# Performance work log

Measured on AMD Instinct MI355X. Metric: run time of the kernel, lower is better.

The kernel has to match this reference:

```python
import jax, jax.numpy as jnp
import numpy as np

BINS = 8
EPS = 1e-12  # torch F.normalize default eps


def _pairwise_scores(matf):
    # torch: input1[a,b]=matf[b]; transpose(0,1)->matf[a]; transpose(-2,-1)->matf[a]^T [M,F]
    # matmul with input1[a,b]=matf[b] -> scores[a,b] = matf[a]^T @ matf[b], shape [M,M]
    bs, F, M = matf.shape
    s = jnp.einsum('afm,bfn->abmn', matf, matf)  # [bs, bs, M, M]
    return s.reshape(bs * bs, M * M)


def _histc_rows(x, bins):
    # torch.histc semantics with min=max=0: range = [row.min(), row.max()],
    # values == max land in the last bin.
    mn = jnp.min(x, axis=1, keepdims=True)
    mx = jnp.max(x, axis=1, keepdims=True)
    denom = jnp.where(mx > mn, mx - mn, jnp.ones_like(mx))
    idx = jnp.clip(jnp.floor((x - mn) / denom * bins).astype(jnp.int32), 0, bins - 1)
    nbs = x.shape[0]
    flat = (idx + (jnp.arange(nbs, dtype=jnp.int32) * bins)[:, None]).ravel()
    h = jnp.zeros(nbs * bins, dtype=x.dtype).at[flat].add(1.0)
    return h.reshape(nbs, bins)


def _l2_normalize(h):
    n = jnp.linalg.norm(h, axis=-1, keepdims=True)
    return h / jnp.maximum(n, EPS)


def setup_inputs() -> dict:
    key = jax.random.key(0)
    k1, k2 = jax.random.split(key)
    bs, F, M = 64, 256, 128
    matf1 = jax.random.normal(k1, (bs, F, M), dtype=jnp.float32)
    matf2 = jax.random.normal(k2, (bs, F, M), dtype=jnp.float32)
    return {"matf1": matf1, "matf2": matf2}


def reference(matf1, matf2):
    # scores are .detach()ed in the original; stop_gradient for faithfulness
    scores1 = jax.lax.stop_gradient(_pairwise_scores(matf1))  # [nbs, M*M]
    scores2 = jax.lax.stop_gradient(_pairwise_scores(matf2))
    h1 = _l2_normalize(_histc_rows(scores1, BINS))  # [nbs, 8]
    h2 = _l2_normalize(_histc_rows(scores2, BINS))
    return jnp.concatenate([h1, h2], axis=-1)  # [nbs, 16]
```

## Files before the change

kernel.cpp:

```cpp
#include <hip/hip_runtime.h>
#include <math.h>

#define BS 64
#define F  256
#define M  128
#define MF (M * F)
#define NBP 1056

typedef unsigned short u16;
typedef _Float16 f16x8 __attribute__((ext_vector_type(8)));
typedef float    f32x16 __attribute__((ext_vector_type(16)));

__global__ __launch_bounds__(256) void convert_f16_kernel(
    const float* __restrict__ m1, const float* __restrict__ m2,
    u16* __restrict__ hT)
{
    __shared__ float tile[64 * M];
    const int mat = blockIdx.x >> 6;
    const int b   = blockIdx.x & 63;
    const int f0  = blockIdx.y * 64;
    const float* src = (mat == 0 ? m1 : m2) + (size_t)b * MF + (size_t)f0 * M;
    const int tid = threadIdx.x;

    const float4* g = (const float4*)src;
    float4* s = (float4*)tile;
    #pragma unroll
    for (int i = 0; i < 8; ++i)
        s[tid + i * 256] = g[tid + i * 256];
    __syncthreads();

    const size_t obase = ((size_t)(mat * BS + b) * 32 + (f0 >> 3)) * 1024;
    #pragma unroll
    for (int it = 0; it < 4; ++it) {
        const int idx = it * 256 + tid;
        const int f8l = idx >> 7;
        const int m   = idx & 127;
        u16 hh[8] __attribute__((aligned(16)));
        #pragma unroll
        for (int j = 0; j < 8; ++j) {
            const float x = tile[(f8l * 8 + j) * M + m];
            const _Float16 h = (_Float16)x;
            hh[j] = __builtin_bit_cast(u16, h);
        }
        *(uint4*)&hT[obase + (size_t)idx * 8] = *(const uint4*)hh;
    }
}


#define LOADB(DST, IT) {                                      \
    const u16* pbk = pb + (IT) * 4096;                        \
    DST[0][0] = *(const f16x8*)(pbk);                         \
    DST[0][1] = *(const f16x8*)(pbk + 256);                   \
    DST[1][0] = *(const f16x8*)(pbk + 2048);                  \
    DST[1][1] = *(const f16x8*)(pbk + 2048 + 256);            \
}

#define MFMA_CHUNK(IT, BF) {                                                                        \
    f16x8 af[4];                                                                                    \
    _Pragma("unroll")                                                                               \
    for (int t = 0; t < 4; ++t)                                                                     \
        af[t] = *(const f16x8*)&lds[(IT) * 4096 + t * 256 + abase];                                 \
    _Pragma("unroll")                                                                               \
    for (int ti = 0; ti < 4; ++ti) {                                                                \
        acc[ti][0] = __builtin_amdgcn_mfma_f32_32x32x16_f16(af[ti], BF[0][0], acc[ti][0], 0, 0, 0); \
        acc[ti][1] = __builtin_amdgcn_mfma_f32_32x32x16_f16(af[ti], BF[0][1], acc[ti][1], 0, 0, 0); \
    }                                                                                               \
    _Pragma("unroll")                                                                               \
    for (int t = 0; t < 4; ++t)                                                                     \
        af[t] = *(const f16x8*)&lds[(IT) * 4096 + 2048 + t * 256 + abase];                          \
    _Pragma("unroll")                                                                               \
    for (int ti = 0; ti < 4; ++ti) {                                                                \
        acc[ti][0] = __builtin_amdgcn_mfma_f32_32x32x16_f16(af[ti], BF[1][0], acc[ti][0], 0, 0, 0); \
        acc[ti][1] = __builtin_amdgcn_mfma_f32_32x32x16_f16(af[ti], BF[1][1], acc[ti][1], 0, 0, 0); \
    }                                                                                               \
}

__global__ __launch_bounds__(256, 2) void gram_hist_mfma(
    const u16* __restrict__ hT, float* __restrict__ out)
{
    __shared__ u16 lds[32768];
    __shared__ float smin[4], smax[4];
    __shared__ int hist[2][8];

    const int tid  = threadIdx.x;
    const int lane = tid & 63;
    const int w    = tid >> 6;

    if (tid < 16) hist[tid >> 3][tid & 7] = 0;

    int p = blockIdx.x, a = 0;
    { int cnt = 32; while (p >= cnt) { p -= cnt; ++a; cnt = (64 - a + 1) >> 1; } }
    const int b1 = a + 2 * p;
    int b2 = b1 + 1;
    const bool b2valid = (b2 <= 63);
    if (!b2valid) b2 = b1;
    const int mat = blockIdx.y;

    const int pp = w >> 1;
    const int c  = w & 1;
    const int l31   = lane & 31;
    const int lhalf = lane >> 5;

    const int bsel = pp ? b2 : b1;
    const u16* pb = hT + (size_t)(mat * BS + bsel) * MF
                  + (size_t)(lhalf * 1024 + c * 512 + l31 * 8);

    const u16* pa = hT + (size_t)(mat * BS + a) * MF + tid * 8;

    const int abase = lhalf * 1024 + l31 * 8;

    f32x16 acc[4][2];
    #pragma unroll
    for (int ti = 0; ti < 4; ++ti)
        #pragma unroll
        for (int u = 0; u < 2; ++u)
            #pragma unroll
            for (int r = 0; r < 16; ++r) acc[ti][u][r] = 0.0f;

    f16x8 bA[2][2], bB[2][2];

    LOADB(bA, 0);

    #pragma unroll
    for (int i = 0; i < 16; ++i) {
        const uint4 v = *(const uint4*)(pa + i * 2048);
        *(uint4*)&lds[(tid + i * 256) * 8] = v;
    }
    __syncthreads();

    #pragma unroll
    for (int itp = 0; itp < 4; ++itp) {
        LOADB(bB, 2 * itp + 1);
        MFMA_CHUNK(2 * itp, bA);
        if (itp < 3) LOADB(bA, 2 * itp + 2);
        MFMA_CHUNK(2 * itp + 1, bB);
    }

    float vmin = acc[0][0][0], vmax = vmin;
    #pragma unroll
    for (int ti = 0; ti < 4; ++ti)
        #pragma unroll
        for (int u = 0; u < 2; ++u)
            #pragma unroll
            for (int r = 0; r < 16; ++r) {
                vmin = fminf(vmin, acc[ti][u][r]);
                vmax = fmaxf(vmax, acc[ti][u][r]);
            }
    #pragma unroll
    for (int off = 1; off < 64; off <<= 1) {
        vmin = fminf(vmin, __shfl_xor(vmin, off, 64));
        vmax = fmaxf(vmax, __shfl_xor(vmax, off, 64));
    }
    if (lane == 0) { smin[w] = vmin; smax[w] = vmax; }
    __syncthreads();
    const float pmn = fminf(smin[pp * 2], smin[pp * 2 + 1]);
    const float pmx = fmaxf(smax[pp * 2], smax[pp * 2 + 1]);
    const float denom = (pmx > pmn) ? (pmx - pmn) : 1.0f;
    const float scale = 8.0f / denom;
    const float bias  = -pmn * scale;

    unsigned w0 = 0, w1 = 0;
    #pragma unroll
    for (int ti = 0; ti < 4; ++ti)
        #pragma unroll
        for (int u = 0; u < 2; ++u)
            #pragma unroll
            for (int r = 0; r < 16; ++r) {
                const float t = fmaf(acc[ti][u][r], scale, bias);
                int k = (int)t;
                k = k > 7 ? 7 : k;
                const unsigned inc = 1u << ((k & 3) * 8);
                if (k < 4) w0 += inc; else w1 += inc;
            }
    unsigned e0 = (w0 & 0xFFu)         | (((w0 >> 8)  & 0xFFu) << 16);
    unsigned e1 = ((w0 >> 16) & 0xFFu) | (((w0 >> 24) & 0xFFu) << 16);
    unsigned e2 = (w1 & 0xFFu)         | (((w1 >> 8)  & 0xFFu) << 16);
    unsigned e3 = ((w1 >> 16) & 0xFFu) | (((w1 >> 24) & 0xFFu) << 16);
    #pragma unroll
    for (int off = 32; off > 0; off >>= 1) {
        e0 += __shfl_down(e0, off, 64);
        e1 += __shfl_down(e1, off, 64);
        e2 += __shfl_down(e2, off, 64);
        e3 += __shfl_down(e3, off, 64);
    }
    if (lane == 0) {
        atomicAdd(&hist[pp][0], (int)(e0 & 0xFFFFu)); atomicAdd(&hist[pp][1], (int)(e0 >> 16));
        atomicAdd(&hist[pp][2], (int)(e1 & 0xFFFFu)); atomicAdd(&hist[pp][3], (int)(e1 >> 16));
        atomicAdd(&hist[pp][4], (int)(e2 & 0xFFFFu)); atomicAdd(&hist[pp][5], (int)(e2 >> 16));
        atomicAdd(&hist[pp][6], (int)(e3 & 0xFFFFu)); atomicAdd(&hist[pp][7], (int)(e3 >> 16));
    }
    __syncthreads();

    const int B = (pp == 0) ? b1 : b2;
    const bool valid = (pp == 0) || b2valid;
    if (valid && c == 0 && lane < 8) {
        float ss = 0.0f;
        #pragma unroll
        for (int k = 0; k < 8; ++k) {
            const float cc = (float)hist[pp][k];
            ss += cc * cc;
        }
        const float nrm = fmaxf(sqrtf(ss), 1e-12f);
        const float v = (float)hist[pp][lane] / nrm;
        out[((size_t)a * BS + B) * 16 + mat * 8 + lane] = v;
        if (a != B)
            out[((size_t)B * BS + a) * 16 + mat * 8 + lane] = v;
    }
}

extern "C" void kernel_launch(void* const* d_in, const int* in_sizes, int n_in,
                              void* d_out, int out_size, void* d_ws, size_t ws_size,
                              hipStream_t stream) {
    const float* m1 = (const float*)d_in[0];
    const float* m2 = (const float*)d_in[1];
    float* out = (float*)d_out;

    u16* hT = (u16*)d_ws;

    convert_f16_kernel<<<dim3(128, 4), 256, 0, stream>>>(m1, m2, hT);
    gram_hist_mfma<<<dim3(NBP, 2), 256, 0, stream>>>(hT, out);
}
```

Before: 116.1 us.

## Double-buffer A tile in LDS and overlap its loads with MFMA compute

Replaces the up-front staging of the full 64KB A matrix into LDS with a 4-phase double-buffered pipeline. Each phase holds 16KB, and the next phase's A and B global loads are issued while the current phase's MFMAs run. This cuts LDS use from 64KB to 32KB per block, which may raise occupancy, and hides the initial load latency. It adds per-phase barriers, sched_barrier fences and s_setprio around the MFMA blocks, and the B register double buffer doubles in size, which increases VGPR pressure.

After: 113.2 us. -2.5%, faster.

```diff
diff --git a/kernel.cpp b/kernel.cpp
--- a/kernel.cpp
+++ b/kernel.cpp
@@ -47,38 +47,62 @@
 }
 
 
-#define LOADB(DST, IT) {                                      \
-    const u16* pbk = pb + (IT) * 4096;                        \
-    DST[0][0] = *(const f16x8*)(pbk);                         \
-    DST[0][1] = *(const f16x8*)(pbk + 256);                   \
-    DST[1][0] = *(const f16x8*)(pbk + 2048);                  \
-    DST[1][1] = *(const f16x8*)(pbk + 2048 + 256);            \
-}
-
-#define MFMA_CHUNK(IT, BF) {                                                                        \
-    f16x8 af[4];                                                                                    \
-    _Pragma("unroll")                                                                               \
-    for (int t = 0; t < 4; ++t)                                                                     \
-        af[t] = *(const f16x8*)&lds[(IT) * 4096 + t * 256 + abase];                                 \
-    _Pragma("unroll")                                                                               \
-    for (int ti = 0; ti < 4; ++ti) {                                                                \
-        acc[ti][0] = __builtin_amdgcn_mfma_f32_32x32x16_f16(af[ti], BF[0][0], acc[ti][0], 0, 0, 0); \
-        acc[ti][1] = __builtin_amdgcn_mfma_f32_32x32x16_f16(af[ti], BF[0][1], acc[ti][1], 0, 0, 0); \
-    }                                                                                               \
-    _Pragma("unroll")                                                                               \
-    for (int t = 0; t < 4; ++t)                                                                     \
-        af[t] = *(const f16x8*)&lds[(IT) * 4096 + 2048 + t * 256 + abase];                          \
-    _Pragma("unroll")                                                                               \
-    for (int ti = 0; ti < 4; ++ti) {                                                                \
-        acc[ti][0] = __builtin_amdgcn_mfma_f32_32x32x16_f16(af[ti], BF[1][0], acc[ti][0], 0, 0, 0); \
-        acc[ti][1] = __builtin_amdgcn_mfma_f32_32x32x16_f16(af[ti], BF[1][1], acc[ti][1], 0, 0, 0); \
-    }                                                                                               \
+#define LOADB(DST, P) {                                               \
+    const u16* pbk = pb + (P) * 8192;                                 \
+    DST[0][0][0] = *(const f16x8*)(pbk);                              \
+    DST[0][0][1] = *(const f16x8*)(pbk + 256);                        \
+    DST[0][1][0] = *(const f16x8*)(pbk + 2048);                       \
+    DST[0][1][1] = *(const f16x8*)(pbk + 2048 + 256);                 \
+    DST[1][0][0] = *(const f16x8*)(pbk + 4096);                       \
+    DST[1][0][1] = *(const f16x8*)(pbk + 4096 + 256);                 \
+    DST[1][1][0] = *(const f16x8*)(pbk + 4096 + 2048);                \
+    DST[1][1][1] = *(const f16x8*)(pbk + 4096 + 2048 + 256);          \
+}
+
+#define LOADA(P) {                                                    \
+    const u16* pak = pa + (P) * 8192;                                 \
+    rA0 = *(const uint4*)(pak);                                       \
+    rA1 = *(const uint4*)(pak + 2048);                                \
+    rA2 = *(const uint4*)(pak + 4096);                                \
+    rA3 = *(const uint4*)(pak + 6144);                                \
+}
+
+#define WRITEA(BUF) {                                                 \
+    *(uint4*)&lds[(BUF) + d0]        = rA0;                           \
+    *(uint4*)&lds[(BUF) + 2048 + d0] = rA1;                           \
+    *(uint4*)&lds[(BUF) + 4096 + d0] = rA2;                           \
+    *(uint4*)&lds[(BUF) + 6144 + d0] = rA3;                           \
+}
+
+#define MFMA_P(CUR, BF) {                                                                               \
+    __builtin_amdgcn_s_setprio(1);                                                                      \
+    _Pragma("unroll")                                                                                   \
+    for (int ITl = 0; ITl < 2; ++ITl) {                                                                 \
+        f16x8 af[4];                                                                                    \
+        _Pragma("unroll")                                                                               \
+        for (int t = 0; t < 4; ++t)                                                                     \
+            af[t] = *(const f16x8*)&lds[(CUR) + ITl * 4096 + t * 256 + abase];                          \
+        _Pragma("unroll")                                                                               \
+        for (int ti = 0; ti < 4; ++ti) {                                                                \
+            acc[ti][0] = __builtin_amdgcn_mfma_f32_32x32x16_f16(af[ti], BF[ITl][0][0], acc[ti][0], 0, 0, 0); \
+            acc[ti][1] = __builtin_amdgcn_mfma_f32_32x32x16_f16(af[ti], BF[ITl][0][1], acc[ti][1], 0, 0, 0); \
+        }                                                                                               \
+        _Pragma("unroll")                                                                               \
+        for (int t = 0; t < 4; ++t)                                                                     \
+            af[t] = *(const f16x8*)&lds[(CUR) + ITl * 4096 + 2048 + t * 256 + abase];                   \
+        _Pragma("unroll")                                                                               \
+        for (int ti = 0; ti < 4; ++ti) {                                                                \
+            acc[ti][0] = __builtin_amdgcn_mfma_f32_32x32x16_f16(af[ti], BF[ITl][1][0], acc[ti][0], 0, 0, 0); \
+            acc[ti][1] = __builtin_amdgcn_mfma_f32_32x32x16_f16(af[ti], BF[ITl][1][1], acc[ti][1], 0, 0, 0); \
+        }                                                                                               \
+    }                                                                                                   \
+    __builtin_amdgcn_s_setprio(0);                                                                      \
 }
 
 __global__ __launch_bounds__(256, 2) void gram_hist_mfma(
     const u16* __restrict__ hT, float* __restrict__ out)
 {
-    __shared__ u16 lds[32768];
+    __shared__ u16 lds[2 * 8192];
     __shared__ float smin[4], smax[4];
     __shared__ int hist[2][8];
 
@@ -101,14 +125,15 @@
     const int l31   = lane & 31;
     const int lhalf = lane >> 5;
 
+    const u16* pa = hT + (size_t)(mat * BS + a) * MF + tid * 8;
+    const int d0 = tid * 8;
+
+    const int abase = lhalf * 1024 + l31 * 8;
+
     const int bsel = pp ? b2 : b1;
     const u16* pb = hT + (size_t)(mat * BS + bsel) * MF
                   + (size_t)(lhalf * 1024 + c * 512 + l31 * 8);
 
-    const u16* pa = hT + (size_t)(mat * BS + a) * MF + tid * 8;
-
-    const int abase = lhalf * 1024 + l31 * 8;
-
     f32x16 acc[4][2];
     #pragma unroll
     for (int ti = 0; ti < 4; ++ti)
@@ -117,24 +142,33 @@
             #pragma unroll
             for (int r = 0; r < 16; ++r) acc[ti][u][r] = 0.0f;
 
-    f16x8 bA[2][2], bB[2][2];
+    uint4 rA0, rA1, rA2, rA3;
+    f16x8 bA[2][2][2], bB[2][2][2];
 
     LOADB(bA, 0);
-
-    #pragma unroll
-    for (int i = 0; i < 16; ++i) {
-        const uint4 v = *(const uint4*)(pa + i * 2048);
-        *(uint4*)&lds[(tid + i * 256) * 8] = v;
-    }
-    __syncthreads();
-
-    #pragma unroll
-    for (int itp = 0; itp < 4; ++itp) {
-        LOADB(bB, 2 * itp + 1);
-        MFMA_CHUNK(2 * itp, bA);
-        if (itp < 3) LOADB(bA, 2 * itp + 2);
-        MFMA_CHUNK(2 * itp + 1, bB);
-    }
+    LOADA(0);
+    WRITEA(0);
+    __syncthreads();
+
+    LOADA(1); LOADB(bB, 1);
+    MFMA_P(0, bA);
+    __builtin_amdgcn_sched_barrier(0);
+    WRITEA(8192);
+    __syncthreads();
+
+    LOADA(2); LOADB(bA, 2);
+    MFMA_P(8192, bB);
+    __builtin_amdgcn_sched_barrier(0);
+    WRITEA(0);
+    __syncthreads();
+
+    LOADA(3); LOADB(bB, 3);
+    MFMA_P(0, bA);
+    __builtin_amdgcn_sched_barrier(0);
+    WRITEA(8192);
+    __syncthreads();
+
+    MFMA_P(8192, bB);
 
     float vmin = acc[0][0][0], vmax = vmin;
     #pragma unroll
```

## Tile gram pairs as 2x2 blocks with double-buffered LDS staging

Applied to the files above, without the earlier changes.

Each workgroup now handles a 2x2 tile of batch pairs (row pair ta, column pair tb) with 512 threads, instead of one row against two columns. Both A and B operands are staged through double-buffered LDS slices, so global loads for the next slice overlap with MFMA work on the current one, and each loaded matrix is reused across two pairs. The change also remaps block indices for scheduling and raises MFMA wave priority. The cost is higher LDS use (128KB per block), which may limit occupancy. Diagonal tiles also compute some redundant pairs.

Result: slower. 127.9 us (+10.2%).

```diff
diff --git a/kernel.cpp b/kernel.cpp
--- a/kernel.cpp
+++ b/kernel.cpp
@@ -5,7 +5,7 @@
 #define F  256
 #define M  128
 #define MF (M * F)
-#define NBP 1056
+#define NTILE 528
 
 typedef unsigned short u16;
 typedef _Float16 f16x8 __attribute__((ext_vector_type(8)));
@@ -47,67 +47,86 @@
 }
 
 
-#define LOADB(DST, IT) {                                      \
-    const u16* pbk = pb + (IT) * 4096;                        \
-    DST[0][0] = *(const f16x8*)(pbk);                         \
-    DST[0][1] = *(const f16x8*)(pbk + 256);                   \
-    DST[1][0] = *(const f16x8*)(pbk + 2048);                  \
-    DST[1][1] = *(const f16x8*)(pbk + 2048 + 256);            \
-}
-
-#define MFMA_CHUNK(IT, BF) {                                                                        \
-    f16x8 af[4];                                                                                    \
-    _Pragma("unroll")                                                                               \
-    for (int t = 0; t < 4; ++t)                                                                     \
-        af[t] = *(const f16x8*)&lds[(IT) * 4096 + t * 256 + abase];                                 \
-    _Pragma("unroll")                                                                               \
-    for (int ti = 0; ti < 4; ++ti) {                                                                \
-        acc[ti][0] = __builtin_amdgcn_mfma_f32_32x32x16_f16(af[ti], BF[0][0], acc[ti][0], 0, 0, 0); \
-        acc[ti][1] = __builtin_amdgcn_mfma_f32_32x32x16_f16(af[ti], BF[0][1], acc[ti][1], 0, 0, 0); \
-    }                                                                                               \
-    _Pragma("unroll")                                                                               \
-    for (int t = 0; t < 4; ++t)                                                                     \
-        af[t] = *(const f16x8*)&lds[(IT) * 4096 + 2048 + t * 256 + abase];                          \
-    _Pragma("unroll")                                                                               \
-    for (int ti = 0; ti < 4; ++ti) {                                                                \
-        acc[ti][0] = __builtin_amdgcn_mfma_f32_32x32x16_f16(af[ti], BF[1][0], acc[ti][0], 0, 0, 0); \
-        acc[ti][1] = __builtin_amdgcn_mfma_f32_32x32x16_f16(af[ti], BF[1][1], acc[ti][1], 0, 0, 0); \
-    }                                                                                               \
-}
-
-__global__ __launch_bounds__(256, 2) void gram_hist_mfma(
+#define SLOAD(S) {                                    \
+    const u16* sp = srcp + (S) * 8192;                \
+    sr0 = *(const uint4*)(sp);                        \
+    sr1 = *(const uint4*)(sp + 1024);                 \
+    sr2 = *(const uint4*)(sp + 2048);                 \
+    sr3 = *(const uint4*)(sp + 3072);                 \
+    sr4 = *(const uint4*)(sp + 4096);                 \
+    sr5 = *(const uint4*)(sp + 5120);                 \
+    sr6 = *(const uint4*)(sp + 6144);                 \
+    sr7 = *(const uint4*)(sp + 7168);                 \
+}
+
+#define SWRITE(BUF) {                                 \
+    u16* dp = &lds[dstb + (BUF)];                     \
+    *(uint4*)(dp)        = sr0;                       \
+    *(uint4*)(dp + 1024) = sr1;                       \
+    *(uint4*)(dp + 2048) = sr2;                       \
+    *(uint4*)(dp + 3072) = sr3;                       \
+    *(uint4*)(dp + 4096) = sr4;                       \
+    *(uint4*)(dp + 5120) = sr5;                       \
+    *(uint4*)(dp + 6144) = sr6;                       \
+    *(uint4*)(dp + 7168) = sr7;                       \
+}
+
+#define MFMA_SLICE(BUF) {                                                                             \
+    __builtin_amdgcn_s_setprio(1);                                                                    \
+    _Pragma("unroll")                                                                                 \
+    for (int ITl = 0; ITl < 2; ++ITl) {                                                               \
+        _Pragma("unroll")                                                                             \
+        for (int kk = 0; kk < 2; ++kk) {                                                              \
+            const int base = (BUF) + ITl * 4096 + kk * 2048;                                          \
+            f16x8 af[4], bf[2];                                                                       \
+            _Pragma("unroll")                                                                         \
+            for (int t = 0; t < 4; ++t)                                                               \
+                af[t] = *(const f16x8*)&lds[base + aoffW + t * 256];                                  \
+            bf[0] = *(const f16x8*)&lds[base + boffW];                                                \
+            bf[1] = *(const f16x8*)&lds[base + boffW + 256];                                          \
+            _Pragma("unroll")                                                                         \
+            for (int ti = 0; ti < 4; ++ti) {                                                          \
+                acc[ti][0] = __builtin_amdgcn_mfma_f32_32x32x16_f16(af[ti], bf[0], acc[ti][0], 0, 0, 0); \
+                acc[ti][1] = __builtin_amdgcn_mfma_f32_32x32x16_f16(af[ti], bf[1], acc[ti][1], 0, 0, 0); \
+            }                                                                                         \
+        }                                                                                             \
+    }                                                                                                 \
+    __builtin_amdgcn_s_setprio(0);                                                                    \
+}
+
+__global__ __launch_bounds__(512, 2) void gram_hist_mfma(
     const u16* __restrict__ hT, float* __restrict__ out)
 {
-    __shared__ u16 lds[32768];
-    __shared__ float smin[4], smax[4];
-    __shared__ int hist[2][8];
+    __shared__ u16 lds[4 * 2 * 8192];
+    __shared__ float smin[8], smax[8];
+    __shared__ int hist[4][8];
 
     const int tid  = threadIdx.x;
     const int lane = tid & 63;
     const int w    = tid >> 6;
 
-    if (tid < 16) hist[tid >> 3][tid & 7] = 0;
-
-    int p = blockIdx.x, a = 0;
-    { int cnt = 32; while (p >= cnt) { p -= cnt; ++a; cnt = (64 - a + 1) >> 1; } }
-    const int b1 = a + 2 * p;
-    int b2 = b1 + 1;
-    const bool b2valid = (b2 <= 63);
-    if (!b2valid) b2 = b1;
+    if (tid < 32) hist[tid >> 3][tid & 7] = 0;
+
+    int x = blockIdx.x;
+    x = (x & 7) * 66 + (x >> 3);
+    int tt = x, ta = 0, cnt = 32;
+    while (tt >= cnt) { tt -= cnt; ++ta; cnt = 32 - ta; }
+    const int tb  = ta + tt;
     const int mat = blockIdx.y;
 
-    const int pp = w >> 1;
+    const int m  = w >> 1;
     const int c  = w & 1;
     const int l31   = lane & 31;
     const int lhalf = lane >> 5;
 
-    const int bsel = pp ? b2 : b1;
-    const u16* pb = hT + (size_t)(mat * BS + bsel) * MF
-                  + (size_t)(lhalf * 1024 + c * 512 + l31 * 8);
-
-    const u16* pa = hT + (size_t)(mat * BS + a) * MF + tid * 8;
-
-    const int abase = lhalf * 1024 + l31 * 8;
+    const int srow = tid >> 7;
+    const int tl   = tid & 127;
+    const int rsel = (srow < 2) ? (2 * ta + srow) : (2 * tb + (srow - 2));
+    const u16* srcp = hT + (size_t)(mat * BS + rsel) * MF + tl * 8;
+    const int dstb = srow * 16384 + tl * 8;
+
+    const int aoffW = (m >> 1) * 16384 + lhalf * 1024 + l31 * 8;
+    const int boffW = (2 + (m & 1)) * 16384 + lhalf * 1024 + c * 512 + l31 * 8;
 
     f32x16 acc[4][2];
     #pragma unroll
@@ -117,24 +136,30 @@
             #pragma unroll
             for (int r = 0; r < 16; ++r) acc[ti][u][r] = 0.0f;
 
-    f16x8 bA[2][2], bB[2][2];
-
-    LOADB(bA, 0);
-
-    #pragma unroll
-    for (int i = 0; i < 16; ++i) {
-        const uint4 v = *(const uint4*)(pa + i * 2048);
-        *(uint4*)&lds[(tid + i * 256) * 8] = v;
-    }
-    __syncthreads();
-
-    #pragma unroll
-    for (int itp = 0; itp < 4; ++itp) {
-        LOADB(bB, 2 * itp + 1);
-        MFMA_CHUNK(2 * itp, bA);
-        if (itp < 3) LOADB(bA, 2 * itp + 2);
-        MFMA_CHUNK(2 * itp + 1, bB);
-    }
+    uint4 sr0, sr1, sr2, sr3, sr4, sr5, sr6, sr7;
+
+    SLOAD(0); SWRITE(0);
+    __syncthreads();
+
+    SLOAD(1);
+    MFMA_SLICE(0);
+    __builtin_amdgcn_sched_barrier(0);
+    SWRITE(8192);
+    __syncthreads();
+
+    SLOAD(2);
+    MFMA_SLICE(8192);
+    __builtin_amdgcn_sched_barrier(0);
+    SWRITE(0);
+    __syncthreads();
+
+    SLOAD(3);
+    MFMA_SLICE(0);
+    __builtin_amdgcn_sched_barrier(0);
+    SWRITE(8192);
+    __syncthreads();
+
+    MFMA_SLICE(8192);
 
     float vmin = acc[0][0][0], vmax = vmin;
     #pragma unroll
@@ -153,8 +178,8 @@
     }
     if (lane == 0) { smin[w] = vmin; smax[w] = vmax; }
     __syncthreads();
-    const float pmn = fminf(smin[pp * 2], smin[pp * 2 + 1]);
-    const float pmx = fmaxf(smax[pp * 2], smax[pp * 2 + 1]);
+    const float pmn = fminf(smin[m * 2], smin[m * 2 + 1]);
+    const float pmx = fmaxf(smax[m * 2], smax[m * 2 + 1]);
     const float denom = (pmx > pmn) ? (pmx - pmn) : 1.0f;
     const float scale = 8.0f / denom;
     const float bias  = -pmn * scale;
@@ -184,27 +209,27 @@
         e3 += __shfl_down(e3, off, 64);
     }
     if (lane == 0) {
-        atomicAdd(&hist[pp][0], (int)(e0 & 0xFFFFu)); atomicAdd(&hist[pp][1], (int)(e0 >> 16));
-        atomicAdd(&hist[pp][2], (int)(e1 & 0xFFFFu)); atomicAdd(&hist[pp][3], (int)(e1 >> 16));
-        atomicAdd(&hist[pp][4], (int)(e2 & 0xFFFFu)); atomicAdd(&hist[pp][5], (int)(e2 >> 16));
-        atomicAdd(&hist[pp][6], (int)(e3 & 0xFFFFu)); atomicAdd(&hist[pp][7], (int)(e3 >> 16));
-    }
-    __syncthreads();
-
-    const int B = (pp == 0) ? b1 : b2;
-    const bool valid = (pp == 0) || b2valid;
-    if (valid && c == 0 && lane < 8) {
+        atomicAdd(&hist[m][0], (int)(e0 & 0xFFFFu)); atomicAdd(&hist[m][1], (int)(e0 >> 16));
+        atomicAdd(&hist[m][2], (int)(e1 & 0xFFFFu)); atomicAdd(&hist[m][3], (int)(e1 >> 16));
+        atomicAdd(&hist[m][4], (int)(e2 & 0xFFFFu)); atomicAdd(&hist[m][5], (int)(e2 >> 16));
+        atomicAdd(&hist[m][6], (int)(e3 & 0xFFFFu)); atomicAdd(&hist[m][7], (int)(e3 >> 16));
+    }
+    __syncthreads();
+
+    if (c == 0 && lane < 8) {
         float ss = 0.0f;
         #pragma unroll
         for (int k = 0; k < 8; ++k) {
-            const float cc = (float)hist[pp][k];
+            const float cc = (float)hist[m][k];
             ss += cc * cc;
         }
         const float nrm = fmaxf(sqrtf(ss), 1e-12f);
-        const float v = (float)hist[pp][lane] / nrm;
-        out[((size_t)a * BS + B) * 16 + mat * 8 + lane] = v;
-        if (a != B)
-            out[((size_t)B * BS + a) * 16 + mat * 8 + lane] = v;
+        const float v = (float)hist[m][lane] / nrm;
+        const int A = 2 * ta + (m >> 1);
+        const int B = 2 * tb + (m & 1);
+        out[((size_t)A * BS + B) * 16 + mat * 8 + lane] = v;
+        if (A != B)
+            out[((size_t)B * BS + A) * 16 + mat * 8 + lane] = v;
     }
 }
 
@@ -218,5 +243,5 @@
     u16* hT = (u16*)d_ws;
 
     convert_f16_kernel<<<dim3(128, 4), 256, 0, stream>>>(m1, m2, hT);
-    gram_hist_mfma<<<dim3(NBP, 2), 256, 0, stream>>>(hT, out);
-}
+    gram_hist_mfma<<<dim3(NTILE, 2), 512, 0, stream>>>(hT, out);
+}
```

## Stream A operand through triple-buffered LDS ring and remap blocks per XCD

Applied to the files above, without the earlier changes.

Rather than loading the whole 64KB A panel into LDS up front, the kernel streams it in 8KB chunks through a three-slot LDS ring. Each chunk is prefetched into registers and written to the next slot while MFMAs run on the current one, and B fragments are prefetched three chunks ahead. It also flattens the grid to 1D and maps blocks so each XCD handles a contiguous range of one matrix, to improve L2 locality. This cuts LDS use from 64KB to 24KB, which could allow higher occupancy, at the cost of a barrier per chunk and more live registers.

New measurement: 119.3 us. 1.03x slower.

```diff
diff --git a/kernel.cpp b/kernel.cpp
--- a/kernel.cpp
+++ b/kernel.cpp
@@ -47,38 +47,54 @@
 }
 
 
-#define LOADB(DST, IT) {                                      \
-    const u16* pbk = pb + (IT) * 4096;                        \
-    DST[0][0] = *(const f16x8*)(pbk);                         \
-    DST[0][1] = *(const f16x8*)(pbk + 256);                   \
-    DST[1][0] = *(const f16x8*)(pbk + 2048);                  \
-    DST[1][1] = *(const f16x8*)(pbk + 2048 + 256);            \
-}
-
-#define MFMA_CHUNK(IT, BF) {                                                                        \
-    f16x8 af[4];                                                                                    \
-    _Pragma("unroll")                                                                               \
-    for (int t = 0; t < 4; ++t)                                                                     \
-        af[t] = *(const f16x8*)&lds[(IT) * 4096 + t * 256 + abase];                                 \
-    _Pragma("unroll")                                                                               \
-    for (int ti = 0; ti < 4; ++ti) {                                                                \
-        acc[ti][0] = __builtin_amdgcn_mfma_f32_32x32x16_f16(af[ti], BF[0][0], acc[ti][0], 0, 0, 0); \
-        acc[ti][1] = __builtin_amdgcn_mfma_f32_32x32x16_f16(af[ti], BF[0][1], acc[ti][1], 0, 0, 0); \
-    }                                                                                               \
-    _Pragma("unroll")                                                                               \
-    for (int t = 0; t < 4; ++t)                                                                     \
-        af[t] = *(const f16x8*)&lds[(IT) * 4096 + 2048 + t * 256 + abase];                          \
-    _Pragma("unroll")                                                                               \
-    for (int ti = 0; ti < 4; ++ti) {                                                                \
-        acc[ti][0] = __builtin_amdgcn_mfma_f32_32x32x16_f16(af[ti], BF[1][0], acc[ti][0], 0, 0, 0); \
-        acc[ti][1] = __builtin_amdgcn_mfma_f32_32x32x16_f16(af[ti], BF[1][1], acc[ti][1], 0, 0, 0); \
-    }                                                                                               \
+#define KBAR() {                                              \
+    asm volatile("s_waitcnt lgkmcnt(0)" ::: "memory");        \
+    __builtin_amdgcn_s_barrier();                             \
+    __builtin_amdgcn_sched_barrier(0);                        \
+}
+
+#define LOADB_S(SLOT, CH) {                                   \
+    const u16* pbk = pb + (CH) * 4096;                        \
+    bF[SLOT][0][0] = *(const f16x8*)(pbk);                    \
+    bF[SLOT][0][1] = *(const f16x8*)(pbk + 256);              \
+    bF[SLOT][1][0] = *(const f16x8*)(pbk + 2048);             \
+    bF[SLOT][1][1] = *(const f16x8*)(pbk + 2048 + 256);       \
+}
+
+#define CHUNK(C) {                                                            \
+    if ((C) <= 5) {                                                           \
+        rA[(C) & 1][0] = *(const uint4*)(pa + ((C) + 2) * 4096);              \
+        rA[(C) & 1][1] = *(const uint4*)(pa + ((C) + 2) * 4096 + 2048);       \
+    }                                                                         \
+    {                                                                         \
+        const int cb = ((C) % 3) * 4096;                                      \
+        _Pragma("unroll")                                                     \
+        for (int kk = 0; kk < 2; ++kk) {                                      \
+            const int base = cb + kk * 2048 + lhalf * 1024 + l31 * 8;         \
+            f16x8 af[4];                                                      \
+            _Pragma("unroll")                                                 \
+            for (int t = 0; t < 4; ++t)                                       \
+                af[t] = *(const f16x8*)&lds[base + t * 256];                  \
+            _Pragma("unroll")                                                 \
+            for (int ti = 0; ti < 4; ++ti) {                                  \
+                acc[ti][0] = __builtin_amdgcn_mfma_f32_32x32x16_f16(af[ti], bF[(C) % 3][kk][0], acc[ti][0], 0, 0, 0); \
+                acc[ti][1] = __builtin_amdgcn_mfma_f32_32x32x16_f16(af[ti], bF[(C) % 3][kk][1], acc[ti][1], 0, 0, 0); \
+            }                                                                 \
+        }                                                                     \
+    }                                                                         \
+    if ((C) <= 4) LOADB_S((C) % 3, (C) + 3);                                  \
+    if ((C) <= 6) {                                                           \
+        const int nb = (((C) + 1) % 3) * 4096;                                \
+        *(uint4*)&lds[nb + d0] = rA[((C) + 1) & 1][0];                        \
+        *(uint4*)&lds[nb + d1] = rA[((C) + 1) & 1][1];                        \
+        KBAR();                                                               \
+    }                                                                         \
 }
 
 __global__ __launch_bounds__(256, 2) void gram_hist_mfma(
     const u16* __restrict__ hT, float* __restrict__ out)
 {
-    __shared__ u16 lds[32768];
+    __shared__ u16 lds[3 * 4096];
     __shared__ float smin[4], smax[4];
     __shared__ int hist[2][8];
 
@@ -88,27 +104,30 @@
 
     if (tid < 16) hist[tid >> 3][tid & 7] = 0;
 
-    int p = blockIdx.x, a = 0;
+    const int bid  = blockIdx.x;
+    const int xcd  = bid & 7;
+    const int mat  = xcd >> 2;
+    int p = (xcd & 3) * 264 + (bid >> 3);
+    int a = 0;
     { int cnt = 32; while (p >= cnt) { p -= cnt; ++a; cnt = (64 - a + 1) >> 1; } }
     const int b1 = a + 2 * p;
     int b2 = b1 + 1;
     const bool b2valid = (b2 <= 63);
     if (!b2valid) b2 = b1;
-    const int mat = blockIdx.y;
 
     const int pp = w >> 1;
     const int c  = w & 1;
     const int l31   = lane & 31;
     const int lhalf = lane >> 5;
 
+    const u16* pa = hT + (size_t)(mat * BS + a) * MF + tid * 8;
+    const int d0 = tid * 8;
+    const int d1 = (256 + tid) * 8;
+
     const int bsel = pp ? b2 : b1;
     const u16* pb = hT + (size_t)(mat * BS + bsel) * MF
                   + (size_t)(lhalf * 1024 + c * 512 + l31 * 8);
 
-    const u16* pa = hT + (size_t)(mat * BS + a) * MF + tid * 8;
-
-    const int abase = lhalf * 1024 + l31 * 8;
-
     f32x16 acc[4][2];
     #pragma unroll
     for (int ti = 0; ti < 4; ++ti)
@@ -117,24 +136,22 @@
             #pragma unroll
             for (int r = 0; r < 16; ++r) acc[ti][u][r] = 0.0f;
 
-    f16x8 bA[2][2], bB[2][2];
-
-    LOADB(bA, 0);
-
-    #pragma unroll
-    for (int i = 0; i < 16; ++i) {
-        const uint4 v = *(const uint4*)(pa + i * 2048);
-        *(uint4*)&lds[(tid + i * 256) * 8] = v;
-    }
-    __syncthreads();
-
-    #pragma unroll
-    for (int itp = 0; itp < 4; ++itp) {
-        LOADB(bB, 2 * itp + 1);
-        MFMA_CHUNK(2 * itp, bA);
-        if (itp < 3) LOADB(bA, 2 * itp + 2);
-        MFMA_CHUNK(2 * itp + 1, bB);
-    }
+    uint4 rA[2][2];
+    f16x8 bF[3][2][2];
+
+    rA[0][0] = *(const uint4*)(pa);
+    rA[0][1] = *(const uint4*)(pa + 2048);
+    rA[1][0] = *(const uint4*)(pa + 4096);
+    rA[1][1] = *(const uint4*)(pa + 4096 + 2048);
+    LOADB_S(0, 0);
+    LOADB_S(1, 1);
+    LOADB_S(2, 2);
+    *(uint4*)&lds[d0] = rA[0][0];
+    *(uint4*)&lds[d1] = rA[0][1];
+    KBAR();
+
+    CHUNK(0); CHUNK(1); CHUNK(2); CHUNK(3);
+    CHUNK(4); CHUNK(5); CHUNK(6); CHUNK(7);
 
     float vmin = acc[0][0][0], vmax = vmin;
     #pragma unroll
@@ -218,5 +235,5 @@
     u16* hT = (u16*)d_ws;
 
     convert_f16_kernel<<<dim3(128, 4), 256, 0, stream>>>(m1, m2, hT);
-    gram_hist_mfma<<<dim3(NBP, 2), 256, 0, stream>>>(hT, out);
-}
+    gram_hist_mfma<<<2 * NBP, 256, 0, stream>>>(hT, out);
+}
```
